# Kernel optimization log

Measured on AMD Instinct MI355X. Metric: run time of the kernel, lower is better.

The kernel has to match this reference:

```python
import jax, jax.numpy as jnp
import numpy as np

N_USERS = 300000
N_ITEMS = 200000
N = N_USERS + N_ITEMS   # total nodes
E = 1250000             # edges
DIM = 64
N_LAYERS = 3


def setup_inputs() -> dict:
    key = jax.random.key(0)
    k1, k2, k3 = jax.random.split(key, 3)
    # xavier-uniform-ish init for embedding table
    bound = float(np.sqrt(6.0 / (N + DIM)))
    embedding = jax.random.uniform(k1, (N, DIM), dtype=jnp.float32, minval=-bound, maxval=bound)
    edge_index = jax.random.randint(k2, (2, E), 0, N, dtype=jnp.int64)
    edge_weight = jax.random.uniform(k3, (E,), dtype=jnp.float32)
    return {"embedding": embedding, "edge_index": edge_index, "edge_weight": edge_weight}


def reference(embedding, edge_index, edge_weight):
    # LightGCN propagation: L layers of gather-scale-scatter_add, mean over layers 0..L
    row, col = edge_index[0], edge_index[1]
    x = embedding
    acc = embedding  # layer-0 embedding contributes to the mean
    for _ in range(N_LAYERS):
        # agg[col] += edge_weight * x[row]  (SpMM over sparse edges)
        msgs = edge_weight[:, None] * x[row]          # [E, DIM]
        x = jax.ops.segment_sum(msgs, col, num_segments=N)  # [N, DIM]
        acc = acc + x
    return acc / jnp.float32(N_LAYERS + 1)
```

## Files before the change

kernel.cpp:

```cpp
#include <hip/hip_runtime.h>


#define NNODES   500000
#define DIMV     64
#define NEDGE    1250000
#define NELEM    (NNODES * DIMV)
#define NELEM4   (NELEM / 4)

#define SCAN_BLK   256
#define SCAN_ITEMS 8
#define SCAN_CHUNK (SCAN_BLK * SCAN_ITEMS)
#define NB1 ((NNODES + SCAN_CHUNK - 1) / SCAN_CHUNK)

static __device__ __forceinline__ unsigned short f2bf(float f) {
    unsigned u = __float_as_uint(f);
    unsigned r = (u + 0x7fffu + ((u >> 16) & 1u)) >> 16;
    return (unsigned short)r;
}
static __device__ __forceinline__ float bflo(unsigned u) {
    return __uint_as_float(u << 16);
}
static __device__ __forceinline__ float bfhi(unsigned u) {
    return __uint_as_float(u & 0xffff0000u);
}

__global__ __launch_bounds__(256) void lgcn_cvt(
    const float4* __restrict__ emb4, unsigned long long* __restrict__ dst)
{
    int i = blockIdx.x * blockDim.x + threadIdx.x;
    int stride = gridDim.x * blockDim.x;
    for (; i < NELEM4; i += stride) {
        float4 v = emb4[i];
        unsigned lo = (unsigned)f2bf(v.x) | ((unsigned)f2bf(v.y) << 16);
        unsigned hi = (unsigned)f2bf(v.z) | ((unsigned)f2bf(v.w) << 16);
        unsigned long long o = (unsigned long long)lo | ((unsigned long long)hi << 32);
        __builtin_nontemporal_store(o, &dst[i]);
    }
}


__global__ __launch_bounds__(256) void lgcn_hist(
    const int* __restrict__ col, int* __restrict__ cnt)
{
    int e = blockIdx.x * blockDim.x + threadIdx.x;
    if (e >= NEDGE) return;
    int c = col[e];
    if ((unsigned)c >= NNODES) return;
    atomicAdd(&cnt[c], 1);
}

__global__ __launch_bounds__(SCAN_BLK) void lgcn_scan1(
    const int* __restrict__ cnt, int* __restrict__ startv, int* __restrict__ bsum)
{
    __shared__ int sh[SCAN_BLK];
    int b = blockIdx.x;
    int base = b * SCAN_CHUNK;
    int tid = threadIdx.x;
    int v[SCAN_ITEMS];
    int local = 0;
    #pragma unroll
    for (int k = 0; k < SCAN_ITEMS; ++k) {
        int idx = base + tid * SCAN_ITEMS + k;
        v[k] = (idx < NNODES) ? cnt[idx] : 0;
        local += v[k];
    }
    sh[tid] = local;
    __syncthreads();
    for (int off = 1; off < SCAN_BLK; off <<= 1) {
        int x = (tid >= off) ? sh[tid - off] : 0;
        __syncthreads();
        sh[tid] += x;
        __syncthreads();
    }
    int run = (tid == 0) ? 0 : sh[tid - 1];
    if (tid == SCAN_BLK - 1) bsum[b] = sh[tid];
    #pragma unroll
    for (int k = 0; k < SCAN_ITEMS; ++k) {
        int idx = base + tid * SCAN_ITEMS + k;
        if (idx < NNODES) startv[idx] = run;
        run += v[k];
    }
}

__global__ __launch_bounds__(SCAN_BLK) void lgcn_scan2(int* __restrict__ bsum)
{
    __shared__ int sh[SCAN_BLK];
    int tid = threadIdx.x;
    sh[tid] = (tid < NB1) ? bsum[tid] : 0;
    __syncthreads();
    for (int off = 1; off < SCAN_BLK; off <<= 1) {
        int x = (tid >= off) ? sh[tid - off] : 0;
        __syncthreads();
        sh[tid] += x;
        __syncthreads();
    }
    if (tid < NB1) bsum[tid] = (tid == 0) ? 0 : sh[tid - 1];
}

__global__ __launch_bounds__(256) void lgcn_scan3(
    int* __restrict__ startv, int* __restrict__ cursor, const int* __restrict__ bsum)
{
    int i = blockIdx.x * blockDim.x + threadIdx.x;
    if (i < NNODES) {
        int s = startv[i] + bsum[i / SCAN_CHUNK];
        startv[i] = s;
        cursor[i] = s;
    }
    if (i == 0) startv[NNODES] = NEDGE;
}

__global__ __launch_bounds__(256) void lgcn_fill(
    const int* __restrict__ row, const int* __restrict__ col,
    const float* __restrict__ w, int* __restrict__ cursor, int2* __restrict__ pairs)
{
    int e = blockIdx.x * blockDim.x + threadIdx.x;
    if (e >= NEDGE) return;
    int c = col[e];
    if ((unsigned)c >= NNODES) return;
    int r = row[e];
    float wt = w[e];
    if ((unsigned)r >= NNODES) { r = 0; wt = 0.f; }
    int p = atomicAdd(&cursor[c], 1);
    pairs[p] = make_int2(r, __float_as_int(wt));
}

template<int MODE>
__global__ __launch_bounds__(256, 4) void lgcn_gather(
    const unsigned short* __restrict__ src16, unsigned short* __restrict__ xout16,
    const float* __restrict__ emb, const unsigned short* __restrict__ x1,
    const unsigned short* __restrict__ x2, float* __restrict__ outp,
    const int2* __restrict__ pairs, const int* __restrict__ startv)
{
    int t = blockIdx.x * blockDim.x + threadIdx.x;
    int wid = t >> 6;
    int lane = t & 63;
    int g = lane >> 3;
    int sub = lane & 7;
    int n = wid * 8 + g;
    if (n >= NNODES) return;

    int s = startv[n];
    int e = startv[n + 1];

    float a0=0.f,a1=0.f,a2=0.f,a3=0.f,a4=0.f,a5=0.f,a6=0.f,a7=0.f;

    for (int i = s; i < e; i += 8) {
        int2 pr[8];
        #pragma unroll
        for (int k = 0; k < 8; ++k) {
            int idx = i + k;
            idx = idx < e ? idx : e - 1;
            pr[k] = pairs[idx];
        }
        uint4 rv[8];
        #pragma unroll
        for (int k = 0; k < 8; ++k) {
            rv[k] = *reinterpret_cast<const uint4*>(
                &src16[(size_t)pr[k].x * DIMV + sub * 8]);
        }
        #pragma unroll
        for (int k = 0; k < 8; ++k) {
            float wk = (i + k < e) ? __int_as_float(pr[k].y) : 0.f;
            a0 = fmaf(wk, bflo(rv[k].x), a0);
            a1 = fmaf(wk, bfhi(rv[k].x), a1);
            a2 = fmaf(wk, bflo(rv[k].y), a2);
            a3 = fmaf(wk, bfhi(rv[k].y), a3);
            a4 = fmaf(wk, bflo(rv[k].z), a4);
            a5 = fmaf(wk, bfhi(rv[k].z), a5);
            a6 = fmaf(wk, bflo(rv[k].w), a6);
            a7 = fmaf(wk, bfhi(rv[k].w), a7);
        }
    }

    const size_t o = (size_t)n * DIMV + sub * 8;
    if (MODE == 2) {
        float4 e0 = *reinterpret_cast<const float4*>(&emb[o]);
        float4 e1 = *reinterpret_cast<const float4*>(&emb[o + 4]);
        uint4 u1 = *reinterpret_cast<const uint4*>(&x1[o]);
        uint4 u2 = *reinterpret_cast<const uint4*>(&x2[o]);
        float4 r0, r1;
        r0.x = (e0.x + bflo(u1.x) + bflo(u2.x) + a0) * 0.25f;
        r0.y = (e0.y + bfhi(u1.x) + bfhi(u2.x) + a1) * 0.25f;
        r0.z = (e0.z + bflo(u1.y) + bflo(u2.y) + a2) * 0.25f;
        r0.w = (e0.w + bfhi(u1.y) + bfhi(u2.y) + a3) * 0.25f;
        r1.x = (e1.x + bflo(u1.z) + bflo(u2.z) + a4) * 0.25f;
        r1.y = (e1.y + bfhi(u1.z) + bfhi(u2.z) + a5) * 0.25f;
        r1.z = (e1.z + bflo(u1.w) + bflo(u2.w) + a6) * 0.25f;
        r1.w = (e1.w + bfhi(u1.w) + bfhi(u2.w) + a7) * 0.25f;
        *reinterpret_cast<float4*>(&outp[o])     = r0;
        *reinterpret_cast<float4*>(&outp[o + 4]) = r1;
    } else {
        unsigned long long lo =
              (unsigned long long)((unsigned)f2bf(a0) | ((unsigned)f2bf(a1) << 16))
            | ((unsigned long long)((unsigned)f2bf(a2) | ((unsigned)f2bf(a3) << 16)) << 32);
        unsigned long long hi =
              (unsigned long long)((unsigned)f2bf(a4) | ((unsigned)f2bf(a5) << 16))
            | ((unsigned long long)((unsigned)f2bf(a6) | ((unsigned)f2bf(a7) << 16)) << 32);
        __builtin_nontemporal_store(lo, reinterpret_cast<unsigned long long*>(&xout16[o]));
        __builtin_nontemporal_store(hi, reinterpret_cast<unsigned long long*>(&xout16[o + 4]));
    }
}


__global__ __launch_bounds__(256) void lgcn_init(
    const float4* __restrict__ emb, float4* __restrict__ acc,
    float4* __restrict__ A, float4* __restrict__ B)
{
    int i = blockIdx.x * blockDim.x + threadIdx.x;
    int stride = gridDim.x * blockDim.x;
    for (; i < NELEM4; i += stride) {
        float4 v = emb[i];
        acc[i] = v;
        A[i]   = v;
        B[i]   = make_float4(0.f, 0.f, 0.f, 0.f);
    }
}

__global__ __launch_bounds__(256) void lgcn_scatter(
    const float* __restrict__ xcur, float* __restrict__ xnext,
    const int* __restrict__ row, const int* __restrict__ col,
    const float* __restrict__ w)
{
    int t = blockIdx.x * blockDim.x + threadIdx.x;
    int e = t >> 4;
    if (e >= NEDGE) return;
    int d = (t & 15) << 2;
    int r = row[e];
    int c = col[e];
    if ((unsigned)r >= NNODES || (unsigned)c >= NNODES) return;
    float wt = w[e];
    const float4 v = *reinterpret_cast<const float4*>(xcur + (size_t)r * DIMV + d);
    float* dst = xnext + (size_t)c * DIMV + d;
    atomicAdd(dst + 0, wt * v.x);
    atomicAdd(dst + 1, wt * v.y);
    atomicAdd(dst + 2, wt * v.z);
    atomicAdd(dst + 3, wt * v.w);
}

__global__ __launch_bounds__(256) void lgcn_addzero(
    float4* __restrict__ acc, const float4* __restrict__ X, float4* __restrict__ Y)
{
    int i = blockIdx.x * blockDim.x + threadIdx.x;
    int stride = gridDim.x * blockDim.x;
    for (; i < NELEM4; i += stride) {
        float4 a = acc[i];
        float4 x = X[i];
        a.x += x.x; a.y += x.y; a.z += x.z; a.w += x.w;
        acc[i] = a;
        Y[i] = make_float4(0.f, 0.f, 0.f, 0.f);
    }
}

__global__ __launch_bounds__(256) void lgcn_final(
    float4* __restrict__ acc, const float4* __restrict__ X)
{
    int i = blockIdx.x * blockDim.x + threadIdx.x;
    int stride = gridDim.x * blockDim.x;
    for (; i < NELEM4; i += stride) {
        float4 a = acc[i];
        float4 x = X[i];
        a.x = (a.x + x.x) * 0.25f;
        a.y = (a.y + x.y) * 0.25f;
        a.z = (a.z + x.z) * 0.25f;
        a.w = (a.w + x.w) * 0.25f;
        acc[i] = a;
    }
}


extern "C" void kernel_launch(void* const* d_in, const int* in_sizes, int n_in,
                              void* d_out, int out_size, void* d_ws, size_t ws_size,
                              hipStream_t stream) {
    const float* emb  = (const float*)d_in[0];
    const int*   eidx = (const int*)d_in[1];
    const float* ew   = (const float*)d_in[2];
    float* acc = (float*)d_out;

    const int* row = eidx;
    const int* col = eidx + NEDGE;

    unsigned short* E16 = (unsigned short*)d_ws;
    unsigned short* X1  = E16 + NELEM;
    unsigned short* X2  = X1 + NELEM;
    int2*  pairs  = (int2*)(X2 + NELEM);
    int*   startv = (int*)(pairs + NEDGE);
    int*   cursor = startv + (NNODES + 1);
    int*   bsum   = cursor + NNODES;
    const size_t needed = (size_t)3 * NELEM * 2 + (size_t)NEDGE * 8
                        + ((size_t)NNODES + 1) * 4 + (size_t)NNODES * 4 + (size_t)NB1 * 4;

    const int EDGE_BLOCKS = (NEDGE + 255) / 256;
    const int NODE_BLOCKS = (NNODES + 255) / 256;
    const int GW_BLOCKS   = (NNODES * 8 + 255) / 256;

    if (ws_size >= needed) {
        lgcn_cvt<<<2048, 256, 0, stream>>>((const float4*)emb, (unsigned long long*)E16);

        hipMemsetAsync(cursor, 0, (size_t)NNODES * 4, stream);
        lgcn_hist<<<EDGE_BLOCKS, 256, 0, stream>>>(col, cursor);
        lgcn_scan1<<<NB1, SCAN_BLK, 0, stream>>>(cursor, startv, bsum);
        lgcn_scan2<<<1, SCAN_BLK, 0, stream>>>(bsum);
        lgcn_scan3<<<NODE_BLOCKS, 256, 0, stream>>>(startv, cursor, bsum);
        lgcn_fill<<<EDGE_BLOCKS, 256, 0, stream>>>(row, col, ew, cursor, pairs);

        lgcn_gather<0><<<GW_BLOCKS, 256, 0, stream>>>(
            E16, X1, nullptr, nullptr, nullptr, nullptr, pairs, startv);
        lgcn_gather<1><<<GW_BLOCKS, 256, 0, stream>>>(
            X1, X2, nullptr, nullptr, nullptr, nullptr, pairs, startv);
        lgcn_gather<2><<<GW_BLOCKS, 256, 0, stream>>>(
            X2, nullptr, emb, X1, X2, acc, pairs, startv);
    } else {
        float* A = (float*)d_ws;
        float* B = A + NELEM;
        const int SC_BLOCKS = (NEDGE * 16 + 255) / 256;
        lgcn_init<<<2048, 256, 0, stream>>>(
            (const float4*)emb, (float4*)acc, (float4*)A, (float4*)B);
        lgcn_scatter<<<SC_BLOCKS, 256, 0, stream>>>(A, B, row, col, ew);
        lgcn_addzero<<<2048, 256, 0, stream>>>((float4*)acc, (const float4*)B, (float4*)A);
        lgcn_scatter<<<SC_BLOCKS, 256, 0, stream>>>(B, A, row, col, ew);
        lgcn_addzero<<<2048, 256, 0, stream>>>((float4*)acc, (const float4*)A, (float4*)B);
        lgcn_scatter<<<SC_BLOCKS, 256, 0, stream>>>(A, B, row, col, ew);
        lgcn_final<<<2048, 256, 0, stream>>>((float4*)acc, (const float4*)B);
    }
}
```

Before: 396.2 us.

## Fuse bf16 conversion with degree histogram; vectorize edge kernels; nontemporal final I/O

Merges the embedding-to-bf16 conversion and the column-degree histogram into one launch, with separate block ranges doing each job so the two independent passes overlap. The histogram and CSR fill kernels now process two edges per thread using int2/float2 loads, and fill writes packed pairs with nontemporal stores. The final layer's loads of emb and x1 and its output stores become nontemporal to avoid polluting cache. This trims launch overhead and memory transactions in the preprocessing stages, at the cost of mixing workloads within one grid.

```diff
diff --git a/kernel.cpp b/kernel.cpp
--- a/kernel.cpp
+++ b/kernel.cpp
@@ -12,6 +12,12 @@
 #define SCAN_CHUNK (SCAN_BLK * SCAN_ITEMS)
 #define NB1 ((NNODES + SCAN_CHUNK - 1) / SCAN_CHUNK)
 
+#define CVT_BLOCKS  1024
+#define EDGE2_BLOCKS ((NEDGE / 2 + 255) / 256)
+
+typedef float  fx4 __attribute__((ext_vector_type(4)));
+typedef unsigned ux4 __attribute__((ext_vector_type(4)));
+
 static __device__ __forceinline__ unsigned short f2bf(float f) {
     unsigned u = __float_as_uint(f);
     unsigned r = (u + 0x7fffu + ((u >> 16) & 1u)) >> 16;
@@ -24,30 +30,29 @@
     return __uint_as_float(u & 0xffff0000u);
 }
 
-__global__ __launch_bounds__(256) void lgcn_cvt(
-    const float4* __restrict__ emb4, unsigned long long* __restrict__ dst)
-{
-    int i = blockIdx.x * blockDim.x + threadIdx.x;
-    int stride = gridDim.x * blockDim.x;
-    for (; i < NELEM4; i += stride) {
-        float4 v = emb4[i];
-        unsigned lo = (unsigned)f2bf(v.x) | ((unsigned)f2bf(v.y) << 16);
-        unsigned hi = (unsigned)f2bf(v.z) | ((unsigned)f2bf(v.w) << 16);
-        unsigned long long o = (unsigned long long)lo | ((unsigned long long)hi << 32);
-        __builtin_nontemporal_store(o, &dst[i]);
-    }
-}
-
-
-__global__ __launch_bounds__(256) void lgcn_hist(
+__global__ __launch_bounds__(256) void lgcn_cvt_hist(
+    const float4* __restrict__ emb4, unsigned long long* __restrict__ dst,
     const int* __restrict__ col, int* __restrict__ cnt)
 {
-    int e = blockIdx.x * blockDim.x + threadIdx.x;
-    if (e >= NEDGE) return;
-    int c = col[e];
-    if ((unsigned)c >= NNODES) return;
-    atomicAdd(&cnt[c], 1);
-}
+    if (blockIdx.x < CVT_BLOCKS) {
+        int i = blockIdx.x * 256 + threadIdx.x;
+        const int stride = CVT_BLOCKS * 256;
+        for (; i < NELEM4; i += stride) {
+            float4 v = emb4[i];
+            unsigned lo = (unsigned)f2bf(v.x) | ((unsigned)f2bf(v.y) << 16);
+            unsigned hi = (unsigned)f2bf(v.z) | ((unsigned)f2bf(v.w) << 16);
+            unsigned long long o = (unsigned long long)lo | ((unsigned long long)hi << 32);
+            __builtin_nontemporal_store(o, &dst[i]);
+        }
+    } else {
+        int t = (blockIdx.x - CVT_BLOCKS) * 256 + threadIdx.x;
+        if (t >= NEDGE / 2) return;
+        int2 c2 = reinterpret_cast<const int2*>(col)[t];
+        if ((unsigned)c2.x < NNODES) atomicAdd(&cnt[c2.x], 1);
+        if ((unsigned)c2.y < NNODES) atomicAdd(&cnt[c2.y], 1);
+    }
+}
+
 
 __global__ __launch_bounds__(SCAN_BLK) void lgcn_scan1(
     const int* __restrict__ cnt, int* __restrict__ startv, int* __restrict__ bsum)
@@ -111,17 +116,31 @@
 
 __global__ __launch_bounds__(256) void lgcn_fill(
     const int* __restrict__ row, const int* __restrict__ col,
-    const float* __restrict__ w, int* __restrict__ cursor, int2* __restrict__ pairs)
-{
-    int e = blockIdx.x * blockDim.x + threadIdx.x;
-    if (e >= NEDGE) return;
-    int c = col[e];
-    if ((unsigned)c >= NNODES) return;
-    int r = row[e];
-    float wt = w[e];
-    if ((unsigned)r >= NNODES) { r = 0; wt = 0.f; }
-    int p = atomicAdd(&cursor[c], 1);
-    pairs[p] = make_int2(r, __float_as_int(wt));
+    const float* __restrict__ w, int* __restrict__ cursor,
+    unsigned long long* __restrict__ pairs)
+{
+    int t = blockIdx.x * blockDim.x + threadIdx.x;
+    if (t >= NEDGE / 2) return;
+    int2   c2 = reinterpret_cast<const int2*>(col)[t];
+    int2   r2 = reinterpret_cast<const int2*>(row)[t];
+    float2 w2 = reinterpret_cast<const float2*>(w)[t];
+
+    if ((unsigned)c2.x < NNODES) {
+        int r = r2.x; float wt = w2.x;
+        if ((unsigned)r >= NNODES) { r = 0; wt = 0.f; }
+        int p = atomicAdd(&cursor[c2.x], 1);
+        unsigned long long pk = (unsigned long long)(unsigned)r
+                              | ((unsigned long long)__float_as_uint(wt) << 32);
+        __builtin_nontemporal_store(pk, &pairs[p]);
+    }
+    if ((unsigned)c2.y < NNODES) {
+        int r = r2.y; float wt = w2.y;
+        if ((unsigned)r >= NNODES) { r = 0; wt = 0.f; }
+        int p = atomicAdd(&cursor[c2.y], 1);
+        unsigned long long pk = (unsigned long long)(unsigned)r
+                              | ((unsigned long long)__float_as_uint(wt) << 32);
+        __builtin_nontemporal_store(pk, &pairs[p]);
+    }
 }
 
 template<int MODE>
@@ -174,11 +193,11 @@
 
     const size_t o = (size_t)n * DIMV + sub * 8;
     if (MODE == 2) {
-        float4 e0 = *reinterpret_cast<const float4*>(&emb[o]);
-        float4 e1 = *reinterpret_cast<const float4*>(&emb[o + 4]);
-        uint4 u1 = *reinterpret_cast<const uint4*>(&x1[o]);
+        fx4 e0 = __builtin_nontemporal_load(reinterpret_cast<const fx4*>(&emb[o]));
+        fx4 e1 = __builtin_nontemporal_load(reinterpret_cast<const fx4*>(&emb[o + 4]));
+        ux4 u1 = __builtin_nontemporal_load(reinterpret_cast<const ux4*>(&x1[o]));
         uint4 u2 = *reinterpret_cast<const uint4*>(&x2[o]);
-        float4 r0, r1;
+        fx4 r0, r1;
         r0.x = (e0.x + bflo(u1.x) + bflo(u2.x) + a0) * 0.25f;
         r0.y = (e0.y + bfhi(u1.x) + bfhi(u2.x) + a1) * 0.25f;
         r0.z = (e0.z + bflo(u1.y) + bflo(u2.y) + a2) * 0.25f;
@@ -187,8 +206,8 @@
         r1.y = (e1.y + bfhi(u1.z) + bfhi(u2.z) + a5) * 0.25f;
         r1.z = (e1.z + bflo(u1.w) + bflo(u2.w) + a6) * 0.25f;
         r1.w = (e1.w + bfhi(u1.w) + bfhi(u2.w) + a7) * 0.25f;
-        *reinterpret_cast<float4*>(&outp[o])     = r0;
-        *reinterpret_cast<float4*>(&outp[o + 4]) = r1;
+        __builtin_nontemporal_store(r0, reinterpret_cast<fx4*>(&outp[o]));
+        __builtin_nontemporal_store(r1, reinterpret_cast<fx4*>(&outp[o + 4]));
     } else {
         unsigned long long lo =
               (unsigned long long)((unsigned)f2bf(a0) | ((unsigned)f2bf(a1) << 16))
@@ -289,19 +308,19 @@
     const size_t needed = (size_t)3 * NELEM * 2 + (size_t)NEDGE * 8
                         + ((size_t)NNODES + 1) * 4 + (size_t)NNODES * 4 + (size_t)NB1 * 4;
 
-    const int EDGE_BLOCKS = (NEDGE + 255) / 256;
     const int NODE_BLOCKS = (NNODES + 255) / 256;
     const int GW_BLOCKS   = (NNODES * 8 + 255) / 256;
 
     if (ws_size >= needed) {
-        lgcn_cvt<<<2048, 256, 0, stream>>>((const float4*)emb, (unsigned long long*)E16);
-
         hipMemsetAsync(cursor, 0, (size_t)NNODES * 4, stream);
-        lgcn_hist<<<EDGE_BLOCKS, 256, 0, stream>>>(col, cursor);
+        lgcn_cvt_hist<<<CVT_BLOCKS + EDGE2_BLOCKS, 256, 0, stream>>>(
+            (const float4*)emb, (unsigned long long*)E16, col, cursor);
+
         lgcn_scan1<<<NB1, SCAN_BLK, 0, stream>>>(cursor, startv, bsum);
         lgcn_scan2<<<1, SCAN_BLK, 0, stream>>>(bsum);
         lgcn_scan3<<<NODE_BLOCKS, 256, 0, stream>>>(startv, cursor, bsum);
-        lgcn_fill<<<EDGE_BLOCKS, 256, 0, stream>>>(row, col, ew, cursor, pairs);
+        lgcn_fill<<<EDGE2_BLOCKS, 256, 0, stream>>>(
+            row, col, ew, cursor, (unsigned long long*)pairs);
 
         lgcn_gather<0><<<GW_BLOCKS, 256, 0, stream>>>(
             E16, X1, nullptr, nullptr, nullptr, nullptr, pairs, startv);
```

Result: faster. 381.6 us (-3.7%).
